# Performance work log

Hardware: AMD Instinct MI355X
Metric: run time of the kernel (lower is better)

## Reference

```python
import jax, jax.numpy as jnp
import numpy as np

COST_CLASS = 1.0
COST_BBOX = 5.0
COST_GIOU = 2.0
EPS = 1e-7


def box_cxcywh_to_xyxy(x):
    cx, cy, w, h = x[..., 0], x[..., 1], x[..., 2], x[..., 3]
    return jnp.stack([cx - 0.5 * w, cy - 0.5 * h, cx + 0.5 * w, cy + 0.5 * h], axis=-1)


def generalized_box_iou(boxes1, boxes2):
    # boxes1: [N,4] xyxy, boxes2: [M,4] xyxy -> [N,M]
    area1 = (boxes1[:, 2] - boxes1[:, 0]) * (boxes1[:, 3] - boxes1[:, 1])
    area2 = (boxes2[:, 2] - boxes2[:, 0]) * (boxes2[:, 3] - boxes2[:, 1])
    lt = jnp.maximum(boxes1[:, None, :2], boxes2[None, :, :2])
    rb = jnp.minimum(boxes1[:, None, 2:], boxes2[None, :, 2:])
    wh = jnp.clip(rb - lt, 0.0)
    inter = wh[..., 0] * wh[..., 1]
    union = area1[:, None] + area2[None, :] - inter
    iou = inter / (union + EPS)
    # smallest enclosing box
    lt_c = jnp.minimum(boxes1[:, None, :2], boxes2[None, :, :2])
    rb_c = jnp.maximum(boxes1[:, None, 2:], boxes2[None, :, 2:])
    wh_c = jnp.clip(rb_c - lt_c, 0.0)
    c_area = wh_c[..., 0] * wh_c[..., 1]
    return iou - (c_area - union) / (c_area + EPS)


def setup_inputs() -> dict:
    key = jax.random.key(0)
    k1, k2, k3, k4 = jax.random.split(key, 4)
    bs, nq, nc, nt = 16, 900, 256, 800
    pred_logits = jax.random.normal(k1, (bs, nq, nc), dtype=jnp.float32)
    pred_boxes = jax.random.uniform(k2, (bs, nq, 4), dtype=jnp.float32)
    tgt_labels = jax.random.randint(k3, (nt,), 0, nc, dtype=jnp.int64)
    tgt_boxes = jax.random.uniform(k4, (nt, 4), dtype=jnp.float32)
    return {"pred_logits": pred_logits, "pred_boxes": pred_boxes,
            "tgt_labels": tgt_labels, "tgt_boxes": tgt_boxes}


def reference(pred_logits, pred_boxes, tgt_labels, tgt_boxes):
    # Returns the full pairwise matching cost tensor C: [bs, num_queries, total_targets].
    # (The scipy linear_sum_assignment / CPU Hungarian step consumes this on host.)
    bs, nq, nc = pred_logits.shape
    out_prob = jax.nn.softmax(pred_logits.reshape(bs * nq, nc), axis=-1)  # [N, nc]
    out_bbox = pred_boxes.reshape(bs * nq, 4)                              # [N, 4]
    cost_class = -out_prob[:, tgt_labels]                                  # [N, M]
    cost_bbox = jnp.abs(out_bbox[:, None, :] - tgt_boxes[None, :, :]).sum(-1)  # L1 cdist [N, M]
    cost_giou = -generalized_box_iou(box_cxcywh_to_xyxy(out_bbox),
                                     box_cxcywh_to_xyxy(tgt_boxes))        # [N, M]
    C = COST_BBOX * cost_bbox + COST_CLASS * cost_class + COST_GIOU * cost_giou
    return C.reshape(bs, nq, -1)
```

## Files before the change

kernel.cpp:

```cpp
#include <hip/hip_runtime.h>
#include <hip/hip_bf16.h>


constexpr float EPS = 1e-7f;

__global__ __launch_bounds__(256) void matcher_kernel(
    const float* __restrict__ logits,
    const float* __restrict__ pboxes,
    const int*   __restrict__ labels,
    const float* __restrict__ tboxes,
    float* __restrict__ out,
    int M, int lbl_mask)
{
    const int n    = blockIdx.x;
    const int tid  = threadIdx.x;
    const int lane = tid & 63;
    const int wave = tid >> 6;

    __shared__ float s_prob[256];
    __shared__ float s_red[4];

    const float x = logits[(size_t)n * 256 + tid];

    float mx = x;
    #pragma unroll
    for (int off = 32; off > 0; off >>= 1)
        mx = fmaxf(mx, __shfl_xor(mx, off, 64));
    if (lane == 0) s_red[wave] = mx;
    __syncthreads();
    mx = fmaxf(fmaxf(s_red[0], s_red[1]), fmaxf(s_red[2], s_red[3]));

    const float e = __expf(x - mx);

    float sum = e;
    #pragma unroll
    for (int off = 32; off > 0; off >>= 1)
        sum += __shfl_xor(sum, off, 64);
    __syncthreads();
    if (lane == 0) s_red[wave] = sum;
    __syncthreads();
    sum = (s_red[0] + s_red[1]) + (s_red[2] + s_red[3]);

    s_prob[tid] = e / sum;
    __syncthreads();

    const float4 pb = reinterpret_cast<const float4*>(pboxes)[n];
    const float ax1 = pb.x - 0.5f * pb.z, ay1 = pb.y - 0.5f * pb.w;
    const float ax2 = pb.x + 0.5f * pb.z, ay2 = pb.y + 0.5f * pb.w;
    const float area1 = (ax2 - ax1) * (ay2 - ay1);

    float* orow = out + (size_t)n * M;
    const int quarters = M >> 2;

    for (int item = tid; item < quarters; item += 256) {
        const int m0 = item * 4;
        float res[4];
        #pragma unroll
        for (int j = 0; j < 4; ++j) {
            const int m = m0 + j;
            const float4 tb = reinterpret_cast<const float4*>(tboxes)[m];
            const float prob = s_prob[labels[m] & lbl_mask];

            const float l1 = fabsf(pb.x - tb.x) + fabsf(pb.y - tb.y)
                           + fabsf(pb.z - tb.z) + fabsf(pb.w - tb.w);

            const float bx1 = tb.x - 0.5f * tb.z, by1 = tb.y - 0.5f * tb.w;
            const float bx2 = tb.x + 0.5f * tb.z, by2 = tb.y + 0.5f * tb.w;
            const float area2 = (bx2 - bx1) * (by2 - by1);

            float iw = fminf(ax2, bx2) - fmaxf(ax1, bx1);
            float ih = fminf(ay2, by2) - fmaxf(ay1, by1);
            iw = fmaxf(iw, 0.0f); ih = fmaxf(ih, 0.0f);
            const float inter = iw * ih;
            const float uni = area1 + area2 - inter;
            const float iou = inter / (uni + EPS);

            float cw = fmaxf(ax2, bx2) - fminf(ax1, bx1);
            float ch = fmaxf(ay2, by2) - fminf(ay1, by1);
            cw = fmaxf(cw, 0.0f); ch = fmaxf(ch, 0.0f);
            const float carea = cw * ch;

            const float giou = iou - (carea - uni) / (carea + EPS);
            res[j] = 5.0f * l1 - prob - 2.0f * giou;
        }
        float4 v = make_float4(res[0], res[1], res[2], res[3]);
        reinterpret_cast<float4*>(orow)[item] = v;
    }

    for (int m = (quarters << 2) + tid; m < M; m += 256) {
        const float4 tb = reinterpret_cast<const float4*>(tboxes)[m];
        const float prob = s_prob[labels[m] & lbl_mask];
        const float l1 = fabsf(pb.x - tb.x) + fabsf(pb.y - tb.y)
                       + fabsf(pb.z - tb.z) + fabsf(pb.w - tb.w);
        const float bx1 = tb.x - 0.5f * tb.z, by1 = tb.y - 0.5f * tb.w;
        const float bx2 = tb.x + 0.5f * tb.z, by2 = tb.y + 0.5f * tb.w;
        const float area2 = (bx2 - bx1) * (by2 - by1);
        float iw = fmaxf(fminf(ax2, bx2) - fmaxf(ax1, bx1), 0.0f);
        float ih = fmaxf(fminf(ay2, by2) - fmaxf(ay1, by1), 0.0f);
        const float inter = iw * ih;
        const float uni = area1 + area2 - inter;
        const float iou = inter / (uni + EPS);
        float cw = fmaxf(fmaxf(ax2, bx2) - fminf(ax1, bx1), 0.0f);
        float ch = fmaxf(fmaxf(ay2, by2) - fminf(ay1, by1), 0.0f);
        const float carea = cw * ch;
        const float giou = iou - (carea - uni) / (carea + EPS);
        orow[m] = 5.0f * l1 - prob - 2.0f * giou;
    }
}

extern "C" void kernel_launch(void* const* d_in, const int* in_sizes, int n_in,
                              void* d_out, int out_size, void* d_ws, size_t ws_size,
                              hipStream_t stream) {
    const float* logits = (const float*)d_in[0];
    const float* pboxes = (const float*)d_in[1];
    const int*   labels = (const int*)d_in[2];
    const float* tboxes = (const float*)d_in[3];

    const int N  = in_sizes[1] / 4;
    const int M  = in_sizes[2];
    const int NC = in_sizes[0] / N;
    const int lbl_mask = NC - 1;

    matcher_kernel<<<N, 256, 0, stream>>>(
        logits, pboxes, labels, tboxes, (float*)d_out, M, lbl_mask);
}
```

Baseline: 105.6 us.

## Map one wave per query row, vectorize softmax, use fast reciprocals

Each 64-lane wave now owns one query row, so a block handles four rows. Softmax runs with per-wave float4 loads and shuffle reductions only, which removes the cross-wave shared-memory reductions and the extra barriers. Labels are loaded as int4. The divisions in IoU and GIoU are replaced with hardware approximate reciprocals, and redundant clamps and area arithmetic are dropped. The trade-offs are slightly lower precision and a loop in which each lane covers 64-strided items instead of 256-strided ones.

```diff
diff --git a/kernel.cpp b/kernel.cpp
--- a/kernel.cpp
+++ b/kernel.cpp
@@ -10,100 +10,102 @@
     const int*   __restrict__ labels,
     const float* __restrict__ tboxes,
     float* __restrict__ out,
-    int M, int lbl_mask)
+    int N, int M, int lbl_mask)
 {
-    const int n    = blockIdx.x;
-    const int tid  = threadIdx.x;
-    const int lane = tid & 63;
-    const int wave = tid >> 6;
+    const int wave = threadIdx.x >> 6;
+    const int lane = threadIdx.x & 63;
+    const int n    = blockIdx.x * 4 + wave;
 
-    __shared__ float s_prob[256];
-    __shared__ float s_red[4];
+    __shared__ float s_prob[4][256];
 
-    const float x = logits[(size_t)n * 256 + tid];
+    if (n < N) {
+        const float4 lg =
+            reinterpret_cast<const float4*>(logits)[(size_t)n * 64 + lane];
 
-    float mx = x;
-    #pragma unroll
-    for (int off = 32; off > 0; off >>= 1)
-        mx = fmaxf(mx, __shfl_xor(mx, off, 64));
-    if (lane == 0) s_red[wave] = mx;
+        float mx = fmaxf(fmaxf(lg.x, lg.y), fmaxf(lg.z, lg.w));
+        #pragma unroll
+        for (int off = 32; off > 0; off >>= 1)
+            mx = fmaxf(mx, __shfl_xor(mx, off, 64));
+
+        const float e0 = __expf(lg.x - mx);
+        const float e1 = __expf(lg.y - mx);
+        const float e2 = __expf(lg.z - mx);
+        const float e3 = __expf(lg.w - mx);
+
+        float s = (e0 + e1) + (e2 + e3);
+        #pragma unroll
+        for (int off = 32; off > 0; off >>= 1)
+            s += __shfl_xor(s, off, 64);
+
+        const float inv = __builtin_amdgcn_rcpf(s);
+        reinterpret_cast<float4*>(&s_prob[wave][0])[lane] =
+            make_float4(e0 * inv, e1 * inv, e2 * inv, e3 * inv);
+    }
     __syncthreads();
-    mx = fmaxf(fmaxf(s_red[0], s_red[1]), fmaxf(s_red[2], s_red[3]));
-
-    const float e = __expf(x - mx);
-
-    float sum = e;
-    #pragma unroll
-    for (int off = 32; off > 0; off >>= 1)
-        sum += __shfl_xor(sum, off, 64);
-    __syncthreads();
-    if (lane == 0) s_red[wave] = sum;
-    __syncthreads();
-    sum = (s_red[0] + s_red[1]) + (s_red[2] + s_red[3]);
-
-    s_prob[tid] = e / sum;
-    __syncthreads();
+    if (n >= N) return;
 
     const float4 pb = reinterpret_cast<const float4*>(pboxes)[n];
     const float ax1 = pb.x - 0.5f * pb.z, ay1 = pb.y - 0.5f * pb.w;
     const float ax2 = pb.x + 0.5f * pb.z, ay2 = pb.y + 0.5f * pb.w;
     const float area1 = (ax2 - ax1) * (ay2 - ay1);
 
-    float* orow = out + (size_t)n * M;
-    const int quarters = M >> 2;
+    const float* sp   = s_prob[wave];
+    float*       orow = out + (size_t)n * M;
+    const int items = M >> 2;
 
-    for (int item = tid; item < quarters; item += 256) {
-        const int m0 = item * 4;
+    for (int item = lane; item < items; item += 64) {
+        const int4 lb = reinterpret_cast<const int4*>(labels)[item];
+        const float4* tbp = reinterpret_cast<const float4*>(tboxes) + item * 4;
+        const int ls[4] = {lb.x, lb.y, lb.z, lb.w};
         float res[4];
         #pragma unroll
         for (int j = 0; j < 4; ++j) {
-            const int m = m0 + j;
-            const float4 tb = reinterpret_cast<const float4*>(tboxes)[m];
-            const float prob = s_prob[labels[m] & lbl_mask];
+            const float4 tb  = tbp[j];
+            const float prob = sp[ls[j] & lbl_mask];
 
             const float l1 = fabsf(pb.x - tb.x) + fabsf(pb.y - tb.y)
                            + fabsf(pb.z - tb.z) + fabsf(pb.w - tb.w);
 
             const float bx1 = tb.x - 0.5f * tb.z, by1 = tb.y - 0.5f * tb.w;
             const float bx2 = tb.x + 0.5f * tb.z, by2 = tb.y + 0.5f * tb.w;
-            const float area2 = (bx2 - bx1) * (by2 - by1);
+            const float area2 = tb.z * tb.w;
 
-            float iw = fminf(ax2, bx2) - fmaxf(ax1, bx1);
-            float ih = fminf(ay2, by2) - fmaxf(ay1, by1);
-            iw = fmaxf(iw, 0.0f); ih = fmaxf(ih, 0.0f);
+            const float iw = fmaxf(fminf(ax2, bx2) - fmaxf(ax1, bx1), 0.0f);
+            const float ih = fmaxf(fminf(ay2, by2) - fmaxf(ay1, by1), 0.0f);
             const float inter = iw * ih;
-            const float uni = area1 + area2 - inter;
-            const float iou = inter / (uni + EPS);
+            const float uni   = area1 + area2 - inter;
+            const float iou   = inter * __builtin_amdgcn_rcpf(uni + EPS);
 
-            float cw = fmaxf(ax2, bx2) - fminf(ax1, bx1);
-            float ch = fmaxf(ay2, by2) - fminf(ay1, by1);
-            cw = fmaxf(cw, 0.0f); ch = fmaxf(ch, 0.0f);
+            const float cw = fmaxf(ax2, bx2) - fminf(ax1, bx1);
+            const float ch = fmaxf(ay2, by2) - fminf(ay1, by1);
             const float carea = cw * ch;
 
-            const float giou = iou - (carea - uni) / (carea + EPS);
+            const float giou =
+                iou - (carea - uni) * __builtin_amdgcn_rcpf(carea + EPS);
             res[j] = 5.0f * l1 - prob - 2.0f * giou;
         }
-        float4 v = make_float4(res[0], res[1], res[2], res[3]);
-        reinterpret_cast<float4*>(orow)[item] = v;
+        reinterpret_cast<float4*>(orow)[item] =
+            make_float4(res[0], res[1], res[2], res[3]);
     }
 
-    for (int m = (quarters << 2) + tid; m < M; m += 256) {
-        const float4 tb = reinterpret_cast<const float4*>(tboxes)[m];
-        const float prob = s_prob[labels[m] & lbl_mask];
+    for (int m = (items << 2) + lane; m < M; m += 64) {
+        const float4 tb  = reinterpret_cast<const float4*>(tboxes)[m];
+        const float prob = sp[labels[m] & lbl_mask];
         const float l1 = fabsf(pb.x - tb.x) + fabsf(pb.y - tb.y)
                        + fabsf(pb.z - tb.z) + fabsf(pb.w - tb.w);
         const float bx1 = tb.x - 0.5f * tb.z, by1 = tb.y - 0.5f * tb.w;
         const float bx2 = tb.x + 0.5f * tb.z, by2 = tb.y + 0.5f * tb.w;
-        const float area2 = (bx2 - bx1) * (by2 - by1);
-        float iw = fmaxf(fminf(ax2, bx2) - fmaxf(ax1, bx1), 0.0f);
-        float ih = fmaxf(fminf(ay2, by2) - fmaxf(ay1, by1), 0.0f);
+        const float area2 = tb.z * tb.w;
+        const float iw = fmaxf(fminf(ax2, bx2) - fmaxf(ax1, bx1), 0.0f);
+        const float ih = fmaxf(fminf(ay2, by2) - fmaxf(ay1, by1), 0.0f);
         const float inter = iw * ih;
-        const float uni = area1 + area2 - inter;
-        const float iou = inter / (uni + EPS);
-        float cw = fmaxf(fmaxf(ax2, bx2) - fminf(ax1, bx1), 0.0f);
-        float ch = fmaxf(fmaxf(ay2, by2) - fminf(ay1, by1), 0.0f);
+        const float uni   = area1 + area2 - inter;
+        const float iou   = inter * __builtin_amdgcn_rcpf(uni + EPS);
+        const float cw = fmaxf(ax2, bx2) - fminf(ax1, bx1);
+        const float ch = fmaxf(ay2, by2) - fminf(ay1, by1);
         const float carea = cw * ch;
-        const float giou = iou - (carea - uni) / (carea + EPS);
+        const float giou =
+            iou - (carea - uni) * __builtin_amdgcn_rcpf(carea + EPS);
         orow[m] = 5.0f * l1 - prob - 2.0f * giou;
     }
 }
@@ -121,6 +123,7 @@
     const int NC = in_sizes[0] / N;
     const int lbl_mask = NC - 1;
 
-    matcher_kernel<<<N, 256, 0, stream>>>(
-        logits, pboxes, labels, tboxes, (float*)d_out, M, lbl_mask);
+    const int grid = (N + 3) / 4;
+    matcher_kernel<<<grid, 256, 0, stream>>>(
+        logits, pboxes, labels, tboxes, (float*)d_out, N, M, lbl_mask);
 }
```

Result: faster. 96.50 us (-8.6%).
